# Kernel optimization log

Measured on AMD Instinct MI355X. Metric: run time of the kernel, lower is better.

Reference implementation:

```python
import jax, jax.numpy as jnp
import numpy as np

NUM_USERS = 100000
NUM_ITEMS = 50000
EMB = 64
N_LAYERS = 3
N_EDGES = 2400000
NEG_SLOPE = 0.01  # torch F.leaky_relu default
EPS = 1e-12       # torch F.normalize default eps


def setup_inputs() -> dict:
    key = jax.random.key(0)
    ks = jax.random.split(key, 9)
    N = NUM_USERS + NUM_ITEMS
    adj_rows = jax.random.randint(ks[0], (N_EDGES,), 0, N, dtype=jnp.int32)
    adj_cols = jax.random.randint(ks[1], (N_EDGES,), 0, N, dtype=jnp.int32)
    # normalized adjacency values are small positive numbers
    adj_vals = jax.random.uniform(ks[2], (N_EDGES,), dtype=jnp.float32) * 0.01
    user_emb = jax.random.normal(ks[3], (NUM_USERS, EMB), dtype=jnp.float32) * 0.1
    item_emb = jax.random.normal(ks[4], (NUM_ITEMS, EMB), dtype=jnp.float32) * 0.1
    gc_w = jax.random.normal(ks[5], (N_LAYERS, EMB, EMB), dtype=jnp.float32) * 0.05
    gc_b = jax.random.normal(ks[6], (N_LAYERS, EMB), dtype=jnp.float32) * 0.01
    bi_w = jax.random.normal(ks[7], (N_LAYERS, EMB, EMB), dtype=jnp.float32) * 0.05
    bi_b = jax.random.normal(ks[8], (N_LAYERS, EMB), dtype=jnp.float32) * 0.01
    return {"adj_rows": adj_rows, "adj_cols": adj_cols, "adj_vals": adj_vals,
            "user_emb": user_emb, "item_emb": item_emb,
            "gc_w": gc_w, "gc_b": gc_b, "bi_w": bi_w, "bi_b": bi_b}


def reference(adj_rows, adj_cols, adj_vals, user_emb, item_emb, gc_w, gc_b, bi_w, bi_b):
    n_users = user_emb.shape[0]
    N = n_users + item_emb.shape[0]
    ego = jnp.concatenate([user_emb, item_emb], axis=0)  # [N, d]
    all_emb = [ego]
    n_layers = gc_w.shape[0]
    for i in range(n_layers):
        # SpMM: side = norm_adj @ ego  (COO gather-scale-scatter)
        side = jax.ops.segment_sum(adj_vals[:, None] * ego[adj_cols],
                                   adj_rows, num_segments=N)  # [N, d]
        sum_emb = jax.nn.leaky_relu(side @ gc_w[i] + gc_b[i], NEG_SLOPE)
        bi_emb = jax.nn.leaky_relu((ego * side) @ bi_w[i] + bi_b[i], NEG_SLOPE)
        ego = sum_emb + bi_emb  # dropout p=0 -> identity (eval mode)
        norm = ego / jnp.maximum(
            jnp.linalg.norm(ego, axis=1, keepdims=True), EPS)
        all_emb.append(norm)
    all_emb = jnp.concatenate(all_emb, axis=1)  # [N, d*(1+L)]
    return all_emb[:n_users], all_emb[n_users:]
```

## Files before the change

kernel.cpp:

```cpp
#include <hip/hip_runtime.h>
#include <hip/hip_bf16.h>

#define NUSERS 100000
#define NITEMS 50000
#define NNODES 150000
#define EMB 64
#define NLAYERS 3
#define NEDGES 2400000
#define NTILES (NNODES / 16)
#define NB 293
#define EPB (NEDGES / 256)

typedef __attribute__((ext_vector_type(8))) short short8;
typedef __attribute__((ext_vector_type(4))) float float4v;

__device__ __forceinline__ float bf2f(unsigned short u) {
    return __uint_as_float((unsigned int)u << 16);
}
__device__ __forceinline__ unsigned short f2bf(float f) {
    unsigned int x = __float_as_uint(f);
    return (unsigned short)((x + 0x7FFFu + ((x >> 16) & 1u)) >> 16);
}
__device__ __forceinline__ float bfl(unsigned int u) { return __uint_as_float(u << 16); }
__device__ __forceinline__ float bfh(unsigned int u) { return __uint_as_float(u & 0xffff0000u); }


__global__ __launch_bounds__(1024) void bucket_count_kernel(
    const int* __restrict__ rows, int* __restrict__ cnt)
{
    __shared__ int hist[NB];
    const int t = threadIdx.x, blk = blockIdx.x;
    for (int i = t; i < NB; i += 1024) hist[i] = 0;
    __syncthreads();
    const int base = blk * EPB;
    for (int i = t; i < EPB; i += 1024)
        atomicAdd(&hist[rows[base + i] >> 9], 1);
    __syncthreads();
    for (int i = t; i < NB; i += 1024) cnt[i * 256 + blk] = hist[i];
}

#define SCAN_TOT (NB * 256)
#define SCAN_CH  74
__global__ __launch_bounds__(1024) void bucket_scan_kernel(int* __restrict__ cnt)
{
    __shared__ int part[1024];
    const int t = threadIdx.x;
    const int lo = t * SCAN_CH;
    int s = 0;
    for (int i = 0; i < SCAN_CH; ++i) {
        int idx = lo + i;
        if (idx < SCAN_TOT) s += cnt[idx];
    }
    part[t] = s; __syncthreads();
    int v = s;
    for (int off = 1; off < 1024; off <<= 1) {
        int add = (t >= off) ? part[t - off] : 0;
        __syncthreads();
        part[t] += add;
        __syncthreads();
    }
    int run = part[t] - v;
    for (int i = 0; i < SCAN_CH; ++i) {
        int idx = lo + i;
        if (idx < SCAN_TOT) {
            int c = cnt[idx];
            cnt[idx] = run;
            run += c;
        }
    }
}

__global__ __launch_bounds__(1024) void bucket_scatter_kernel(
    const int* __restrict__ rows, const int* __restrict__ cols,
    const float* __restrict__ vals, const int* __restrict__ offs,
    int2* __restrict__ staged)
{
    __shared__ int cur[NB];
    const int t = threadIdx.x, blk = blockIdx.x;
    for (int i = t; i < NB; i += 1024) cur[i] = offs[i * 256 + blk];
    __syncthreads();
    const int base = blk * EPB;
    for (int i = t; i < EPB; i += 1024) {
        int e = base + i;
        int r = rows[e];
        int pos = atomicAdd(&cur[r >> 9], 1);
        staged[pos] = make_int2(((r & 511) << 18) | cols[e], __float_as_int(vals[e]));
    }
}

__global__ __launch_bounds__(1024) void bucket_csr_kernel(
    const int* __restrict__ offs, const int2* __restrict__ staged,
    int* __restrict__ rowptr, int2* __restrict__ edges)
{
    __shared__ int deg[512];
    __shared__ int cur[512];
    __shared__ int part[256];
    const int t = threadIdx.x, b = blockIdx.x;
    const int bstart = offs[b * 256];
    const int bend   = (b + 1 < NB) ? offs[(b + 1) * 256] : NEDGES;
    if (t < 512) deg[t] = 0;
    __syncthreads();
    for (int i = bstart + t; i < bend; i += 1024)
        atomicAdd(&deg[staged[i].x >> 18], 1);
    __syncthreads();
    int d0 = 0, d1 = 0, s = 0;
    if (t < 256) {
        d0 = deg[2 * t]; d1 = deg[2 * t + 1];
        s = d0 + d1;
        part[t] = s;
    }
    __syncthreads();
    int v = s;
    for (int off = 1; off < 256; off <<= 1) {
        int add = (t >= off && t < 256) ? part[t - off] : 0;
        __syncthreads();
        if (t < 256) part[t] += add;
        __syncthreads();
    }
    if (t < 256) {
        int ex = part[t] - v;
        cur[2 * t]     = ex;
        cur[2 * t + 1] = ex + d0;
        int grow = b * 512 + 2 * t;
        if (grow < NNODES)     rowptr[grow]     = bstart + ex;
        if (grow + 1 < NNODES) rowptr[grow + 1] = bstart + ex + d0;
        if (b == 0 && t == 0)  rowptr[NNODES] = NEDGES;
    }
    __syncthreads();
    for (int i = bstart + t; i < bend; i += 1024) {
        int2 se = staged[i];
        int pos = atomicAdd(&cur[se.x >> 18], 1);
        edges[bstart + pos] = make_int2(se.x & 0x3FFFF, se.y);
    }
}

__global__ __launch_bounds__(256) void wconv_kernel(
    const float* __restrict__ gw, const float* __restrict__ bw,
    unsigned short* __restrict__ wg_bf, unsigned short* __restrict__ wb_bf)
{
    int i = blockIdx.x * 256 + threadIdx.x;
    if (i >= NLAYERS * EMB * EMB) return;
    int l = i >> 12;
    int k = (i >> 6) & 63;
    int n = i & 63;
    int o = (l << 12) | (n << 6) | k;
    wg_bf[o] = f2bf(gw[i]);
    wb_bf[o] = f2bf(bw[i]);
}

__global__ __launch_bounds__(256) void init_kernel(
    const float* __restrict__ ue, const float* __restrict__ ie,
    unsigned short* __restrict__ ego_bf, float* __restrict__ out)
{
    int i = blockIdx.x * 256 + threadIdx.x;
    if (i >= NNODES * 16) return;
    int n = i >> 4, q = i & 15;
    float4 v = (n < NUSERS) ? ((const float4*)ue)[i]
                            : ((const float4*)ie)[i - NUSERS * 16];
    *(float4*)(out + (size_t)n * 256 + q * 4) = v;
    ushort4 b;
    b.x = f2bf(v.x); b.y = f2bf(v.y); b.z = f2bf(v.z); b.w = f2bf(v.w);
    *(ushort4*)(ego_bf + (size_t)n * EMB + q * 4) = b;
}

__global__ __launch_bounds__(256) void spmm_pull(
    const int* __restrict__ rowptr, const int2* __restrict__ edges,
    const unsigned short* __restrict__ ego_bf, unsigned short* __restrict__ side_bf)
{
    const int t  = threadIdx.x;
    const int cp = t & 15;
    const int r  = blockIdx.x * 16 + (t >> 4);
    const int s = rowptr[r], e = rowptr[r + 1];

    float a0 = 0.f, a1 = 0.f, a2 = 0.f, a3 = 0.f;
    float b0 = 0.f, b1 = 0.f, b2 = 0.f, b3 = 0.f;
    int i = s;
    for (; i + 4 <= e; i += 4) {
        int2 e0 = edges[i],     e1 = edges[i + 1];
        int2 e2 = edges[i + 2], e3 = edges[i + 3];
        uint2 u0 = *(const uint2*)(ego_bf + (size_t)e0.x * EMB + cp * 4);
        uint2 u1 = *(const uint2*)(ego_bf + (size_t)e1.x * EMB + cp * 4);
        uint2 u2 = *(const uint2*)(ego_bf + (size_t)e2.x * EMB + cp * 4);
        uint2 u3 = *(const uint2*)(ego_bf + (size_t)e3.x * EMB + cp * 4);
        float v0 = __int_as_float(e0.y), v1 = __int_as_float(e1.y);
        float v2 = __int_as_float(e2.y), v3 = __int_as_float(e3.y);
        a0 += v0 * bfl(u0.x); a1 += v0 * bfh(u0.x);
        a2 += v0 * bfl(u0.y); a3 += v0 * bfh(u0.y);
        b0 += v1 * bfl(u1.x); b1 += v1 * bfh(u1.x);
        b2 += v1 * bfl(u1.y); b3 += v1 * bfh(u1.y);
        a0 += v2 * bfl(u2.x); a1 += v2 * bfh(u2.x);
        a2 += v2 * bfl(u2.y); a3 += v2 * bfh(u2.y);
        b0 += v3 * bfl(u3.x); b1 += v3 * bfh(u3.x);
        b2 += v3 * bfl(u3.y); b3 += v3 * bfh(u3.y);
    }
    for (; i < e; ++i) {
        int2 e0 = edges[i];
        float v0 = __int_as_float(e0.y);
        uint2 u0 = *(const uint2*)(ego_bf + (size_t)e0.x * EMB + cp * 4);
        a0 += v0 * bfl(u0.x); a1 += v0 * bfh(u0.x);
        a2 += v0 * bfl(u0.y); a3 += v0 * bfh(u0.y);
    }
    a0 += b0; a1 += b1; a2 += b2; a3 += b3;

    ushort4 o;
    o.x = f2bf(a0); o.y = f2bf(a1); o.z = f2bf(a2); o.w = f2bf(a3);
    *(ushort4*)(side_bf + (size_t)r * EMB + cp * 4) = o;
}

__global__ __launch_bounds__(256) void dense_mfma(
    const unsigned short* __restrict__ side_bf, unsigned short* __restrict__ ego_bf,
    const unsigned short* __restrict__ wg_bf, const unsigned short* __restrict__ wb_bf,
    const float* __restrict__ gb, const float* __restrict__ bb,
    float* __restrict__ out, int out_col0)
{
    const int lane = threadIdx.x & 63;
    const int w    = threadIdx.x >> 6;
    const int m    = lane & 15;
    const int q    = lane >> 4;

    const int t = (int)blockIdx.x * 4 + w;
    if (t >= NTILES) return;

    short8 bg[4][2], bbf[4][2];
    #pragma unroll
    for (int n0 = 0; n0 < 4; ++n0) {
        const int n = n0 * 16 + m;
        #pragma unroll
        for (int kh = 0; kh < 2; ++kh) {
            bg [n0][kh] = *(const short8*)(wg_bf + n * EMB + kh * 32 + q * 8);
            bbf[n0][kh] = *(const short8*)(wb_bf + n * EMB + kh * 32 + q * 8);
        }
    }
    float bgc[4], bbc[4];
    #pragma unroll
    for (int n0 = 0; n0 < 4; ++n0) { bgc[n0] = gb[n0 * 16 + m]; bbc[n0] = bb[n0 * 16 + m]; }

    const size_t base = (size_t)t * 16 * EMB;
    const int ao = m * EMB + q * 8;
    short8 as0 = *(const short8*)(side_bf + base + ao);
    short8 as1 = *(const short8*)(side_bf + base + ao + 32);
    short8 ae0 = *(const short8*)(ego_bf  + base + ao);
    short8 ae1 = *(const short8*)(ego_bf  + base + ao + 32);
    short8 ap0, ap1;
    #pragma unroll
    for (int jj = 0; jj < 8; ++jj) {
        ap0[jj] = (short)f2bf(bf2f((unsigned short)as0[jj]) * bf2f((unsigned short)ae0[jj]));
        ap1[jj] = (short)f2bf(bf2f((unsigned short)as1[jj]) * bf2f((unsigned short)ae1[jj]));
    }

    float4v c1[4], c2[4];
    #pragma unroll
    for (int n0 = 0; n0 < 4; ++n0) { c1[n0] = (float4v)0.f; c2[n0] = (float4v)0.f; }
    #pragma unroll
    for (int n0 = 0; n0 < 4; ++n0) {
        c1[n0] = __builtin_amdgcn_mfma_f32_16x16x32_bf16(as0, bg [n0][0], c1[n0], 0, 0, 0);
        c1[n0] = __builtin_amdgcn_mfma_f32_16x16x32_bf16(as1, bg [n0][1], c1[n0], 0, 0, 0);
        c2[n0] = __builtin_amdgcn_mfma_f32_16x16x32_bf16(ap0, bbf[n0][0], c2[n0], 0, 0, 0);
        c2[n0] = __builtin_amdgcn_mfma_f32_16x16x32_bf16(ap1, bbf[n0][1], c2[n0], 0, 0, 0);
    }

    float eg[4][4];
    float ss[4] = {0.f, 0.f, 0.f, 0.f};
    #pragma unroll
    for (int n0 = 0; n0 < 4; ++n0) {
        #pragma unroll
        for (int r = 0; r < 4; ++r) {
            float x1 = c1[n0][r] + bgc[n0];
            float x2 = c2[n0][r] + bbc[n0];
            float v1 = x1 > 0.f ? x1 : 0.01f * x1;
            float v2 = x2 > 0.f ? x2 : 0.01f * x2;
            float e = v1 + v2;
            eg[n0][r] = e;
            ss[r] += e * e;
        }
    }
    #pragma unroll
    for (int r = 0; r < 4; ++r) {
        float s = ss[r];
        s += __shfl_xor(s, 1, 64);
        s += __shfl_xor(s, 2, 64);
        s += __shfl_xor(s, 4, 64);
        s += __shfl_xor(s, 8, 64);
        ss[r] = 1.0f / fmaxf(sqrtf(s), 1e-12f);
    }
    #pragma unroll
    for (int r = 0; r < 4; ++r) {
        int row = t * 16 + q * 4 + r;
        #pragma unroll
        for (int n0 = 0; n0 < 4; ++n0) {
            int col = n0 * 16 + m;
            ego_bf[(size_t)row * EMB + col] = f2bf(eg[n0][r]);
            out[(size_t)row * 256 + out_col0 + col] = eg[n0][r] * ss[r];
        }
    }
}

extern "C" void kernel_launch(void* const* d_in, const int* in_sizes, int n_in,
                              void* d_out, int out_size, void* d_ws, size_t ws_size,
                              hipStream_t stream)
{
    const int*   rows = (const int*)  d_in[0];
    const int*   cols = (const int*)  d_in[1];
    const float* vals = (const float*)d_in[2];
    const float* ue   = (const float*)d_in[3];
    const float* ie   = (const float*)d_in[4];
    const float* gw   = (const float*)d_in[5];
    const float* gb   = (const float*)d_in[6];
    const float* bw   = (const float*)d_in[7];
    const float* bb   = (const float*)d_in[8];
    float* out = (float*)d_out;

    char* p = (char*)d_ws;
    unsigned short* ego_bf  = (unsigned short*)p;  p += (size_t)NNODES * EMB * 2;
    unsigned short* side_bf = (unsigned short*)p;  p += (size_t)NNODES * EMB * 2;
    int2*  edges  = (int2*)p;    p += (size_t)NEDGES * 8;
    int*   rowptr = (int*)p;     p += ((size_t)NNODES + 4) * 4;
    unsigned short* wg_bf = (unsigned short*)p;  p += (size_t)NLAYERS * EMB * EMB * 2;
    unsigned short* wb_bf = (unsigned short*)p;  p += (size_t)NLAYERS * EMB * EMB * 2;
    int*   cnt    = (int*)p;     p += (size_t)NB * 256 * 4;
    int2* staged = (int2*)side_bf;

    bucket_count_kernel  <<<256, 1024, 0, stream>>>(rows, cnt);
    bucket_scan_kernel   <<<1,   1024, 0, stream>>>(cnt);
    bucket_scatter_kernel<<<256, 1024, 0, stream>>>(rows, cols, vals, cnt, staged);
    bucket_csr_kernel    <<<NB,  1024, 0, stream>>>(cnt, staged, rowptr, edges);

    wconv_kernel<<<(NLAYERS * EMB * EMB + 255) / 256, 256, 0, stream>>>(gw, bw, wg_bf, wb_bf);
    init_kernel<<<(NNODES * 16 + 255) / 256, 256, 0, stream>>>(ue, ie, ego_bf, out);

    for (int l = 0; l < NLAYERS; ++l) {
        spmm_pull<<<NNODES / 16, 256, 0, stream>>>(rowptr, edges, ego_bf, side_bf);
        dense_mfma<<<(NTILES + 3) / 4, 256, 0, stream>>>(
            side_bf, ego_bf,
            wg_bf + l * EMB * EMB, wb_bf + l * EMB * EMB,
            gb + l * EMB, bb + l * EMB,
            out, 64 * (l + 1));
    }
}
```

Baseline: 642.0 us.

## Replace single-block bucket scan with three-phase parallel scan

The exclusive scan over the per-bucket, per-block edge counts ran in one 1024-thread block with strided serial chunks. It is now split into three stages: a per-bucket reduction across many blocks, a small single-block scan of the bucket totals, and a per-bucket block scan that adds the bucket base. This removes a serial, poorly coalesced bottleneck in CSR construction, at the cost of two extra kernel launches and a small extra workspace buffer.

```diff
diff --git a/kernel.cpp b/kernel.cpp
--- a/kernel.cpp
+++ b/kernel.cpp
@@ -39,35 +39,48 @@
     for (int i = t; i < NB; i += 1024) cnt[i * 256 + blk] = hist[i];
 }
 
-#define SCAN_TOT (NB * 256)
-#define SCAN_CH  74
-__global__ __launch_bounds__(1024) void bucket_scan_kernel(int* __restrict__ cnt)
-{
-    __shared__ int part[1024];
+__global__ __launch_bounds__(256) void bucket_sum_kernel(
+    const int* __restrict__ cnt, int* __restrict__ bsum)
+{
+    __shared__ int ws[4];
+    const int b = blockIdx.x, t = threadIdx.x;
+    int v = cnt[b * 256 + t];
+    #pragma unroll
+    for (int off = 1; off < 64; off <<= 1) v += __shfl_xor(v, off, 64);
+    if ((t & 63) == 0) ws[t >> 6] = v;
+    __syncthreads();
+    if (t == 0) bsum[b] = ws[0] + ws[1] + ws[2] + ws[3];
+}
+
+__global__ __launch_bounds__(512) void bucket_base_kernel(int* __restrict__ bsum)
+{
+    __shared__ int lds[512];
     const int t = threadIdx.x;
-    const int lo = t * SCAN_CH;
-    int s = 0;
-    for (int i = 0; i < SCAN_CH; ++i) {
-        int idx = lo + i;
-        if (idx < SCAN_TOT) s += cnt[idx];
-    }
-    part[t] = s; __syncthreads();
-    int v = s;
-    for (int off = 1; off < 1024; off <<= 1) {
-        int add = (t >= off) ? part[t - off] : 0;
-        __syncthreads();
-        part[t] += add;
-        __syncthreads();
-    }
-    int run = part[t] - v;
-    for (int i = 0; i < SCAN_CH; ++i) {
-        int idx = lo + i;
-        if (idx < SCAN_TOT) {
-            int c = cnt[idx];
-            cnt[idx] = run;
-            run += c;
-        }
-    }
+    int v = (t < NB) ? bsum[t] : 0;
+    lds[t] = v; __syncthreads();
+    for (int off = 1; off < 512; off <<= 1) {
+        int add = (t >= off) ? lds[t - off] : 0;
+        __syncthreads();
+        lds[t] += add;
+        __syncthreads();
+    }
+    if (t < NB) bsum[t] = lds[t] - v;
+}
+
+__global__ __launch_bounds__(256) void bucket_offs_kernel(
+    int* __restrict__ cnt, const int* __restrict__ bsum)
+{
+    __shared__ int lds[256];
+    const int b = blockIdx.x, t = threadIdx.x;
+    int v = cnt[b * 256 + t];
+    lds[t] = v; __syncthreads();
+    for (int off = 1; off < 256; off <<= 1) {
+        int add = (t >= off) ? lds[t - off] : 0;
+        __syncthreads();
+        lds[t] += add;
+        __syncthreads();
+    }
+    cnt[b * 256 + t] = lds[t] - v + bsum[b];
 }
 
 __global__ __launch_bounds__(1024) void bucket_scatter_kernel(
@@ -318,10 +331,13 @@
     unsigned short* wg_bf = (unsigned short*)p;  p += (size_t)NLAYERS * EMB * EMB * 2;
     unsigned short* wb_bf = (unsigned short*)p;  p += (size_t)NLAYERS * EMB * EMB * 2;
     int*   cnt    = (int*)p;     p += (size_t)NB * 256 * 4;
+    int*   bsum   = (int*)p;     p += (size_t)512 * 4;
     int2* staged = (int2*)side_bf;
 
     bucket_count_kernel  <<<256, 1024, 0, stream>>>(rows, cnt);
-    bucket_scan_kernel   <<<1,   1024, 0, stream>>>(cnt);
+    bucket_sum_kernel    <<<NB,  256,  0, stream>>>(cnt, bsum);
+    bucket_base_kernel   <<<1,   512,  0, stream>>>(bsum);
+    bucket_offs_kernel   <<<NB,  256,  0, stream>>>(cnt, bsum);
     bucket_scatter_kernel<<<256, 1024, 0, stream>>>(rows, cols, vals, cnt, staged);
     bucket_csr_kernel    <<<NB,  1024, 0, stream>>>(cnt, staged, rowptr, edges);
 
```

New measurement: 517.6 us. -19.4%, faster.
